# Kernel tuning notes

Measured on AMD Instinct MI355X. Metric: run time of the kernel, lower is better.

Reference implementation:

```python
import jax, jax.numpy as jnp
from jax import lax
import numpy as np

B, L, C = 16, 4096, 512
G = 8            # n_groups
CG = C // G      # group_dim = 64
WD = 4           # weather_dim
ORF = 10.0       # offset_range_factor


def conv1d(x, w, b=None):
    # x: [N, Cin, L], w: [Cout, Cin, 3], stride 1, padding 1
    y = lax.conv_general_dilated(x, w, window_strides=(1,), padding=[(1, 1)],
                                 dimension_numbers=('NCH', 'OIH', 'NCH'))
    if b is not None:
        y = y + b[None, :, None]
    return y


def group_norm(x, gamma, beta, groups=4, eps=1e-5):
    N, Cc, Ln = x.shape
    xr = x.reshape(N, groups, Cc // groups, Ln)
    mu = xr.mean(axis=(2, 3), keepdims=True)
    var = ((xr - mu) ** 2).mean(axis=(2, 3), keepdims=True)
    xn = ((xr - mu) / jnp.sqrt(var + eps)).reshape(N, Cc, Ln)
    return xn * gamma[None, :, None] + beta[None, :, None]


def grid_sample_bilinear_border(inp, grid):
    # Faithful torch F.grid_sample(mode='bilinear', padding_mode='border', align_corners=True)
    # inp: [N, C, H, W]; grid: [N, Ho, Wo, 2], grid[...,0]=x (width coord), grid[...,1]=y (height coord)
    N, Cc, H, W = inp.shape
    _, Ho, Wo, _ = grid.shape
    gx, gy = grid[..., 0], grid[..., 1]
    ix = jnp.clip((gx + 1.0) * 0.5 * (W - 1), 0.0, W - 1)  # border padding clamps coords
    iy = jnp.clip((gy + 1.0) * 0.5 * (H - 1), 0.0, H - 1)
    ix0f = jnp.floor(ix); iy0f = jnp.floor(iy)
    wx = ix - ix0f; wy = iy - iy0f
    ix0 = jnp.clip(ix0f.astype(jnp.int32), 0, W - 1)
    iy0 = jnp.clip(iy0f.astype(jnp.int32), 0, H - 1)
    ix1 = jnp.clip(ix0 + 1, 0, W - 1)
    iy1 = jnp.clip(iy0 + 1, 0, H - 1)
    flat = inp.reshape(N, Cc, H * W)
    def gather(iyk, ixk):
        idx = (iyk * W + ixk).reshape(N, 1, Ho * Wo)
        return jnp.take_along_axis(flat, idx, axis=2).reshape(N, Cc, Ho, Wo)
    v00 = gather(iy0, ix0); v01 = gather(iy0, ix1)
    v10 = gather(iy1, ix0); v11 = gather(iy1, ix1)
    wx = wx[:, None, :, :]; wy = wy[:, None, :, :]
    return (v00 * (1 - wy) * (1 - wx) + v01 * (1 - wy) * wx
            + v10 * wy * (1 - wx) + v11 * wy * wx)


def _forward(x, x_ext, w1, b1, gn_g, gn_b, w2, b2, w3, gate):
    xt = jnp.transpose(x, (0, 2, 1))              # [B, C, L]
    xg = xt.reshape(B * G, CG, L)                 # [B*G, CG, L]
    xe = jnp.transpose(x_ext, (0, 2, 1))          # [B, WD, L]
    xe = jnp.tile(xe, (G, 1, 1))                  # torch .repeat(n_groups,1,1)
    pin = jnp.concatenate([xg, xe], axis=1)       # [B*G, CG+WD, L]
    h = jax.nn.gelu(group_norm(conv1d(pin, w1, b1), gn_g, gn_b), approximate=False)
    h = jax.nn.gelu(conv1d(h, w2, b2), approximate=False)
    offset = jnp.tanh(conv1d(h, w3)) * ORF        # [B*G, 1, L]
    off_n = offset * (2.0 / (L - 1.0))
    ref = (jnp.linspace(0.5, L - 0.5, L, dtype=x.dtype) / (L - 1.0)) * 2.0 - 1.0
    grid_x = jnp.clip(ref[None, None, :, None] + off_n[..., None], -1.0, 1.0)  # [B*G,1,L,1]
    grid = jnp.concatenate([grid_x, jnp.zeros_like(grid_x)], axis=-1)
    grid = jnp.transpose(grid, (0, 2, 1, 3))      # [B*G, L, 1, 2]
    xs = grid_sample_bilinear_border(xg[..., None], grid)[..., 0]  # [B*G, CG, L]
    x_out = xg + jnp.tanh(gate) * xs
    x_out = x_out.reshape(B, C, L)
    return jnp.transpose(x_out, (0, 2, 1)), offset


def setup_inputs() -> dict:
    key = jax.random.key(0)
    ks = jax.random.split(key, 8)
    s = 0.05
    return {
        'x': jax.random.normal(ks[0], (B, L, C), jnp.float32),
        'x_ext': jax.random.normal(ks[1], (B, L, WD), jnp.float32),
        'w1': jax.random.normal(ks[2], (64, CG + WD, 3), jnp.float32) * s,
        'b1': jax.random.normal(ks[3], (64,), jnp.float32) * s,
        'gn_g': jnp.ones((64,), jnp.float32),
        'gn_b': jnp.zeros((64,), jnp.float32),
        'w2': jax.random.normal(ks[4], (32, 64, 3), jnp.float32) * s,
        'b2': jax.random.normal(ks[5], (32,), jnp.float32) * s,
        'w3': jax.random.normal(ks[6], (1, 32, 3), jnp.float32) * s,
        'gate': jnp.array([0.5], jnp.float32),
    }


def reference(x, x_ext, w1, b1, gn_g, gn_b, w2, b2, w3, gate):
    return _forward(x, x_ext, w1, b1, gn_g, gn_b, w2, b2, w3, gate)
```

## Files before the change

### kernel.cpp

```cpp
#include <hip/hip_runtime.h>
#include <hip/hip_bf16.h>

#define BB 16
#define LL 4096
#define CC 512
#define NG 128
#define IC1 68
#define OC1 64
#define OC2 32

typedef short short8 __attribute__((ext_vector_type(8)));
typedef float f32x4 __attribute__((ext_vector_type(4)));

__device__ inline ushort f2b(float f) {
    __hip_bfloat16 h = __float2bfloat16(f);
    return *reinterpret_cast<ushort*>(&h);
}
__device__ inline float b2f(ushort u) {
    __hip_bfloat16 h;
    *reinterpret_cast<ushort*>(&h) = u;
    return __bfloat162float(h);
}
__device__ inline float fast_tanh(float y) {
    float e = __expf(2.0f * y);
    return 1.0f - 2.0f / (e + 1.0f);
}
__device__ inline float fast_gelu(float x) {
    float y = x * (0.7978845608f + 0.0356774081f * x * x);
    return 0.5f * x * (1.0f + fast_tanh(y));
}

__global__ __launch_bounds__(256) void k_prep(const float* __restrict__ x,
    const float* __restrict__ w1, const float* __restrict__ w2,
    const float* __restrict__ gate,
    ushort* __restrict__ w1b, ushort* __restrict__ w2b, float* __restrict__ corr)
{
    int idx = blockIdx.x * 256 + threadIdx.x;
    if (idx < 18432) {
        int k = idx / 6144; int r = idx - k * 6144;
        int oc = r / 96;    int icp = r - oc * 96;
        float v = (icp < IC1) ? w1[(oc * IC1 + icp) * 3 + k] : 0.0f;
        w1b[idx] = f2b(v);
    } else if (idx < 24576) {
        int j = idx - 18432;
        int k = j / 2048; int r = j - k * 2048;
        int oc = r / 64;  int ic = r - oc * 64;
        w2b[j] = f2b(w2[(oc * OC1 + ic) * 3 + k]);
    } else if (idx < 32768) {
        int i3 = idx - 24576;
        int b = i3 >> 9; int ch = i3 & 511;
        float tg = tanhf(gate[0]);
        corr[i3] = tg * 0.5f *
            (x[((size_t)(b * LL + 2047)) * CC + ch] +
             x[((size_t)(b * LL + 2048)) * CC + ch]);
    }
}

#define KA_ROWS 66
#define KA_STR  104
template<bool FULL>
__device__ __forceinline__ void ka_body(ushort* pin,
    const float* __restrict__ x, const float* __restrict__ xe,
    const float* __restrict__ b1, const ushort* __restrict__ w1b,
    float* __restrict__ part, int n, int lt)
{
    const int b = n >> 3, g = n & 7, be = n & 15;
    const int l0 = lt * 64;
    const int t = threadIdx.x;
    const int q = t & 15;

    {
        const float* xb = &x[((size_t)b * LL + (l0 - 1)) * CC + g * 64 + q * 4];
#pragma unroll
        for (int i = 0; i < 9; ++i) {
            int pos = t + i * 128;
            if (pos < KA_ROWS * 16) {
                int li = pos >> 4;
                float4 v;
                if (FULL) {
                    v = *(const float4*)(xb + (size_t)li * CC);
                } else {
                    int l = l0 - 1 + li;
                    v = make_float4(0.f, 0.f, 0.f, 0.f);
                    if (l >= 0 && l < LL) v = *(const float4*)(xb + (size_t)li * CC);
                }
                uint lo = (uint)f2b(v.x) | ((uint)f2b(v.y) << 16);
                uint hi = (uint)f2b(v.z) | ((uint)f2b(v.w) << 16);
                *(uint2*)&pin[li * KA_STR + q * 4] = make_uint2(lo, hi);
            }
        }
    }
    if (t < KA_ROWS) {
        int l = l0 - 1 + t;
        float4 v = make_float4(0.f, 0.f, 0.f, 0.f);
        if (FULL || (l >= 0 && l < LL))
            v = *(const float4*)&xe[(size_t)(be * LL + l) * 4];
        uint lo = (uint)f2b(v.x) | ((uint)f2b(v.y) << 16);
        uint hi = (uint)f2b(v.z) | ((uint)f2b(v.w) << 16);
        *(uint2*)&pin[t * KA_STR + 64] = make_uint2(lo, hi);
    }
#pragma unroll
    for (int i = 0; i < 4; ++i) {
        int pos = t + i * 128;
        if (pos < KA_ROWS * 7) {
            int li = pos / 7, j = pos - li * 7;
            *(uint2*)&pin[li * KA_STR + 68 + j * 4] = make_uint2(0u, 0u);
        }
    }
    __syncthreads();

    const int lane = t & 63;
    const int w = t >> 6;
    const int m = lane & 15, h = lane >> 4;

    short8 fa[2][9];
#pragma unroll
    for (int mi = 0; mi < 2; ++mi)
#pragma unroll
        for (int k = 0; k < 3; ++k)
#pragma unroll
            for (int c = 0; c < 3; ++c)
                fa[mi][k * 3 + c] = *(const short8*)&w1b[
                    (size_t)(k * 64 + w * 32 + mi * 16 + m) * 96 + c * 32 + h * 8];

    f32x4 acc[2][4] = {};
#pragma unroll
    for (int tt = 0; tt < 4; ++tt) {
        const int rowbase = tt * 16 + m;
#pragma unroll
        for (int k = 0; k < 3; ++k) {
#pragma unroll
            for (int c = 0; c < 3; ++c) {
                short8 fb = *(const short8*)&pin[(rowbase + k) * KA_STR + c * 32 + h * 8];
                acc[0][tt] = __builtin_amdgcn_mfma_f32_16x16x32_bf16(fa[0][k * 3 + c], fb, acc[0][tt], 0, 0, 0);
                acc[1][tt] = __builtin_amdgcn_mfma_f32_16x16x32_bf16(fa[1][k * 3 + c], fb, acc[1][tt], 0, 0, 0);
            }
        }
    }

#pragma unroll
    for (int mi = 0; mi < 2; ++mi) {
        float bias[4];
#pragma unroll
        for (int r = 0; r < 4; ++r)
            bias[r] = b1[w * 32 + mi * 16 + h * 4 + r];
        float s1 = 0.f, s2 = 0.f;
#pragma unroll
        for (int tt = 0; tt < 4; ++tt) {
            float v0 = acc[mi][tt][0] + bias[0];
            float v1 = acc[mi][tt][1] + bias[1];
            float v2 = acc[mi][tt][2] + bias[2];
            float v3 = acc[mi][tt][3] + bias[3];
            s1 += v0 + v1 + v2 + v3;
            s2 += v0 * v0 + v1 * v1 + v2 * v2 + v3 * v3;
        }
#pragma unroll
        for (int off = 32; off > 0; off >>= 1) {
            s1 += __shfl_down(s1, off, 64);
            s2 += __shfl_down(s2, off, 64);
        }
        if (lane == 0) {
            int gidx = w * 2 + mi;
            part[(((size_t)n * 4 + gidx) * 64 + lt) * 2 + 0] = s1;
            part[(((size_t)n * 4 + gidx) * 64 + lt) * 2 + 1] = s2;
        }
    }
}

__global__ __launch_bounds__(128, 6) void ka_stats(const float* __restrict__ x,
    const float* __restrict__ xe, const float* __restrict__ b1,
    const ushort* __restrict__ w1b, float* __restrict__ part)
{
    __shared__ ushort pin[KA_ROWS * KA_STR];
    const int n = blockIdx.y, lt = blockIdx.x;
    if (lt >= 1 && lt <= 62)
        ka_body<true>(pin, x, xe, b1, w1b, part, n, lt);
    else
        ka_body<false>(pin, x, xe, b1, w1b, part, n, lt);
}

#define BT 60
#define XR 66
#define PINS 104
#define P2S  72
#define H2S  66
template<bool FULL>
__device__ __forceinline__ void kb_body(ushort* smem, float* sstats,
    const float* __restrict__ x, const float* __restrict__ xe,
    const float* __restrict__ b1, const ushort* __restrict__ w1b,
    const float* __restrict__ part, const float* __restrict__ gn_g,
    const float* __restrict__ gn_b, const float* __restrict__ b2,
    const ushort* __restrict__ w2b, const float* __restrict__ w3,
    const float* __restrict__ corr, float* __restrict__ out,
    float* __restrict__ offs, int n, int lt)
{
    ushort* pin = smem;
    ushort* p2  = smem;
    ushort* h2b = smem + 4752;
    const int b = n >> 3, g = n & 7, be = n & 15;
    const int l0 = lt * BT;
    const int t = threadIdx.x;
    const int lane = t & 63;
    const int w = t >> 6;

#pragma unroll
    for (int gg = 0; gg < 2; ++gg) {
        int gidx = w * 2 + gg;
        float2 p = *(const float2*)&part[(((size_t)n * 4 + gidx) * 64 + lane) * 2];
        float s1 = p.x, s2 = p.y;
#pragma unroll
        for (int off = 32; off > 0; off >>= 1) {
            s1 += __shfl_down(s1, off, 64);
            s2 += __shfl_down(s2, off, 64);
        }
        if (lane == 0) {
            float mean = s1 * (1.0f / 65536.0f);
            float var  = s2 * (1.0f / 65536.0f) - mean * mean;
            sstats[gidx * 2 + 0] = mean;
            sstats[gidx * 2 + 1] = 1.0f / sqrtf(var + 1e-5f);
        }
    }

    const int q = t & 15;
    {
        const float4 corrv = *(const float4*)&corr[(b << 9) + g * 64 + q * 4];
        const float* xb = &x[((size_t)b * LL + (l0 - 3)) * CC + g * 64 + q * 4];
        float* ob = &out[((size_t)b * LL + (l0 - 3)) * CC + g * 64 + q * 4];
#pragma unroll
        for (int i = 0; i < 9; ++i) {
            int pos = t + i * 128;
            if (pos < XR * 16) {
                int li = pos >> 4;
                float4 v;
                bool inr = true;
                if (FULL) {
                    v = *(const float4*)(xb + (size_t)li * CC);
                } else {
                    int l = l0 - 3 + li;
                    inr = (l >= 0 && l < LL);
                    v = make_float4(0.f, 0.f, 0.f, 0.f);
                    if (inr) v = *(const float4*)(xb + (size_t)li * CC);
                }
                if (li >= 3 && li < 3 + BT && inr) {
                    float4 o;
                    o.x = v.x + corrv.x; o.y = v.y + corrv.y;
                    o.z = v.z + corrv.z; o.w = v.w + corrv.w;
                    *(float4*)(ob + (size_t)li * CC) = o;
                }
                uint lo = (uint)f2b(v.x) | ((uint)f2b(v.y) << 16);
                uint hi = (uint)f2b(v.z) | ((uint)f2b(v.w) << 16);
                *(uint2*)&pin[li * PINS + q * 4] = make_uint2(lo, hi);
            }
        }
        if (t < XR) {
            int l = l0 - 3 + t;
            float4 v = make_float4(0.f, 0.f, 0.f, 0.f);
            if (FULL || (l >= 0 && l < LL))
                v = *(const float4*)&xe[(size_t)(be * LL + l) * 4];
            uint lo = (uint)f2b(v.x) | ((uint)f2b(v.y) << 16);
            uint hi = (uint)f2b(v.z) | ((uint)f2b(v.w) << 16);
            *(uint2*)&pin[t * PINS + 64] = make_uint2(lo, hi);
        }
#pragma unroll
        for (int i = 0; i < 4; ++i) {
            int pos = t + i * 128;
            if (pos < XR * 7) {
                int li = pos / 7, j = pos - li * 7;
                *(uint2*)&pin[li * PINS + 68 + j * 4] = make_uint2(0u, 0u);
            }
        }
    }
    __syncthreads();

    const int m = lane & 15, h = lane >> 4;

    short8 fa[2][9];
#pragma unroll
    for (int mi = 0; mi < 2; ++mi)
#pragma unroll
        for (int k = 0; k < 3; ++k)
#pragma unroll
            for (int c = 0; c < 3; ++c)
                fa[mi][k * 3 + c] = *(const short8*)&w1b[
                    (size_t)(k * 64 + w * 32 + mi * 16 + m) * 96 + c * 32 + h * 8];

    f32x4 acc[2][4] = {};
#pragma unroll
    for (int tt = 0; tt < 4; ++tt) {
        const int rowbase = tt * 16 + m;
#pragma unroll
        for (int k = 0; k < 3; ++k) {
#pragma unroll
            for (int c = 0; c < 3; ++c) {
                short8 fb = *(const short8*)&pin[(rowbase + k) * PINS + c * 32 + h * 8];
                acc[0][tt] = __builtin_amdgcn_mfma_f32_16x16x32_bf16(fa[0][k * 3 + c], fb, acc[0][tt], 0, 0, 0);
                acc[1][tt] = __builtin_amdgcn_mfma_f32_16x16x32_bf16(fa[1][k * 3 + c], fb, acc[1][tt], 0, 0, 0);
            }
        }
    }
    __syncthreads();

#pragma unroll
    for (int mi = 0; mi < 2; ++mi) {
        int gi = w * 2 + mi;
        float mean = sstats[gi * 2], istd = sstats[gi * 2 + 1];
        float A_[4], B_[4];
#pragma unroll
        for (int r = 0; r < 4; ++r) {
            int oc = w * 32 + mi * 16 + h * 4 + r;
            float ga = gn_g[oc];
            A_[r] = istd * ga;
            B_[r] = gn_b[oc] + (b1[oc] - mean) * A_[r];
        }
#pragma unroll
        for (int tt = 0; tt < 4; ++tt) {
            int p = tt * 16 + m;
            uint2 pk = make_uint2(0u, 0u);
            int l = l0 - 2 + p;
            if (FULL || (l >= 0 && l < LL)) {
                float v0 = fast_gelu(fmaf(acc[mi][tt][0], A_[0], B_[0]));
                float v1 = fast_gelu(fmaf(acc[mi][tt][1], A_[1], B_[1]));
                float v2 = fast_gelu(fmaf(acc[mi][tt][2], A_[2], B_[2]));
                float v3 = fast_gelu(fmaf(acc[mi][tt][3], A_[3], B_[3]));
                pk.x = (uint)f2b(v0) | ((uint)f2b(v1) << 16);
                pk.y = (uint)f2b(v2) | ((uint)f2b(v3) << 16);
            }
            *(uint2*)&p2[p * P2S + w * 32 + mi * 16 + h * 4] = pk;
        }
    }
    __syncthreads();

    short8 fa2[6];
#pragma unroll
    for (int k = 0; k < 3; ++k)
#pragma unroll
        for (int c = 0; c < 2; ++c)
            fa2[k * 2 + c] = *(const short8*)&w2b[
                (size_t)(k * 32 + w * 16 + m) * 64 + c * 32 + h * 8];

    float bias2[4];
#pragma unroll
    for (int r = 0; r < 4; ++r)
        bias2[r] = b2[w * 16 + h * 4 + r];

    f32x4 acc2[4] = {};
#pragma unroll
    for (int u = 0; u < 4; ++u) {
        const int jb = u * 16 + m;
#pragma unroll
        for (int k = 0; k < 3; ++k) {
#pragma unroll
            for (int c = 0; c < 2; ++c) {
                short8 fb = *(const short8*)&p2[(jb + k) * P2S + c * 32 + h * 8];
                acc2[u] = __builtin_amdgcn_mfma_f32_16x16x32_bf16(fa2[k * 2 + c], fb, acc2[u], 0, 0, 0);
            }
        }
    }
#pragma unroll
    for (int u = 0; u < 4; ++u) {
        int j = u * 16 + m;
        int lj = l0 - 1 + j;
#pragma unroll
        for (int r = 0; r < 4; ++r) {
            int oc = w * 16 + h * 4 + r;
            float v = 0.f;
            if (FULL || (lj >= 0 && lj < LL))
                v = fast_gelu(acc2[u][r] + bias2[r]);
            h2b[oc * H2S + j] = f2b(v);
        }
    }
    __syncthreads();

    if (t < 2 * BT) {
        int qq = t >> 1, half = t & 1;
        int ic0 = half * 16;
        float a = 0.f;
#pragma unroll
        for (int ic = 0; ic < 16; ++ic) {
            int icc = ic0 + ic;
            float v0 = b2f(h2b[icc * H2S + qq]);
            float v1 = b2f(h2b[icc * H2S + qq + 1]);
            float v2 = b2f(h2b[icc * H2S + qq + 2]);
            a = fmaf(w3[icc * 3 + 0], v0, a);
            a = fmaf(w3[icc * 3 + 1], v1, a);
            a = fmaf(w3[icc * 3 + 2], v2, a);
        }
        a += __shfl_xor(a, 1, 64);
        if (half == 0) {
            int l = l0 + qq;
            if (FULL || l < LL)
                offs[(size_t)n * LL + l] = fast_tanh(a) * 10.0f;
        }
    }
}

__global__ __launch_bounds__(128, 6) void kb_fused(const float* __restrict__ x,
    const float* __restrict__ xe, const float* __restrict__ b1,
    const ushort* __restrict__ w1b, const float* __restrict__ part,
    const float* __restrict__ gn_g, const float* __restrict__ gn_b,
    const float* __restrict__ b2, const ushort* __restrict__ w2b,
    const float* __restrict__ w3, const float* __restrict__ corr,
    float* __restrict__ out, float* __restrict__ offs)
{
    __shared__ ushort smem[6864];
    __shared__ float sstats[8];
    const int n = blockIdx.y, lt = blockIdx.x;
    if (lt >= 1 && lt <= 67)
        kb_body<true >(smem, sstats, x, xe, b1, w1b, part, gn_g, gn_b, b2, w2b, w3, corr, out, offs, n, lt);
    else
        kb_body<false>(smem, sstats, x, xe, b1, w1b, part, gn_g, gn_b, b2, w2b, w3, corr, out, offs, n, lt);
}

extern "C" void kernel_launch(void* const* d_in, const int* in_sizes, int n_in,
                              void* d_out, int out_size, void* d_ws, size_t ws_size,
                              hipStream_t stream)
{
    const float* x    = (const float*)d_in[0];
    const float* xext = (const float*)d_in[1];
    const float* w1   = (const float*)d_in[2];
    const float* b1   = (const float*)d_in[3];
    const float* gng  = (const float*)d_in[4];
    const float* gnb  = (const float*)d_in[5];
    const float* w2   = (const float*)d_in[6];
    const float* b2   = (const float*)d_in[7];
    const float* w3   = (const float*)d_in[8];
    const float* gate = (const float*)d_in[9];

    float* out  = (float*)d_out;
    float* offs = out + (size_t)BB * LL * CC;

    char* ws = (char*)d_ws;
    float* part = (float*)(ws);
    ushort* w1b = (ushort*)(ws + 262144);
    ushort* w2b = (ushort*)(ws + 299008);
    float* corr = (float*)(ws + 311296);

    k_prep<<<128, 256, 0, stream>>>(x, w1, w2, gate, w1b, w2b, corr);
    dim3 g1(64, NG);
    ka_stats<<<g1, 128, 0, stream>>>(x, xext, b1, w1b, part);
    dim3 g3(69, NG);
    kb_fused<<<g3, 128, 0, stream>>>(x, xext, b1, w1b, part, gng, gnb, b2, w2b,
                                     w3, corr, out, offs);
}
```

Measured before the change: 186.1 us.

## Write output and bf16 x copy in stats pass; read compact bf16 in fused pass

The stats kernel now covers 128 positions with 256 threads and, while loading x, also writes the residual output (x + corr) and a compact per-group bf16 copy of x to workspace. The fused kernel then reads that bf16 copy instead of re-reading fp32 x, and uses an XOR-swizzled LDS layout with separate storage for the weather channels. Moving the output write into the first pass and halving the second pass's x read volume is meant to cut global traffic. In exchange it adds an extra bf16 write and read through workspace, and relaxes the fused kernel's launch bounds.

Result: faster. 166.8 us (-10.4%).

```diff
diff --git a/kernel.cpp b/kernel.cpp
--- a/kernel.cpp
+++ b/kernel.cpp
@@ -56,24 +56,28 @@
     }
 }
 
-#define KA_ROWS 66
+#define KA_ROWS 130
 #define KA_STR  104
 template<bool FULL>
 __device__ __forceinline__ void ka_body(ushort* pin,
     const float* __restrict__ x, const float* __restrict__ xe,
     const float* __restrict__ b1, const ushort* __restrict__ w1b,
-    float* __restrict__ part, int n, int lt)
+    const float* __restrict__ corr, float* __restrict__ part,
+    float* __restrict__ out, ushort* __restrict__ xbf, int n, int lt)
 {
     const int b = n >> 3, g = n & 7, be = n & 15;
-    const int l0 = lt * 64;
+    const int l0 = lt * 128;
     const int t = threadIdx.x;
     const int q = t & 15;
 
     {
+        const float4 corrv = *(const float4*)&corr[(b << 9) + g * 64 + q * 4];
         const float* xb = &x[((size_t)b * LL + (l0 - 1)) * CC + g * 64 + q * 4];
+        float* ob = &out[((size_t)b * LL + (l0 - 1)) * CC + g * 64 + q * 4];
+        ushort* xbb = &xbf[((size_t)n * LL + (l0 - 1)) * 64 + q * 4];
 #pragma unroll
         for (int i = 0; i < 9; ++i) {
-            int pos = t + i * 128;
+            int pos = t + i * 256;
             if (pos < KA_ROWS * 16) {
                 int li = pos >> 4;
                 float4 v;
@@ -86,7 +90,15 @@
                 }
                 uint lo = (uint)f2b(v.x) | ((uint)f2b(v.y) << 16);
                 uint hi = (uint)f2b(v.z) | ((uint)f2b(v.w) << 16);
-                *(uint2*)&pin[li * KA_STR + q * 4] = make_uint2(lo, hi);
+                uint2 pk = make_uint2(lo, hi);
+                if (li >= 1 && li <= 128) {
+                    float4 o;
+                    o.x = v.x + corrv.x; o.y = v.y + corrv.y;
+                    o.z = v.z + corrv.z; o.w = v.w + corrv.w;
+                    *(float4*)(ob + (size_t)li * CC) = o;
+                    *(uint2*)(xbb + (size_t)li * 64) = pk;
+                }
+                *(uint2*)&pin[li * KA_STR + q * 4] = pk;
             }
         }
     }
@@ -101,7 +113,7 @@
     }
 #pragma unroll
     for (int i = 0; i < 4; ++i) {
-        int pos = t + i * 128;
+        int pos = t + i * 256;
         if (pos < KA_ROWS * 7) {
             int li = pos / 7, j = pos - li * 7;
             *(uint2*)&pin[li * KA_STR + 68 + j * 4] = make_uint2(0u, 0u);
@@ -111,6 +123,7 @@
 
     const int lane = t & 63;
     const int w = t >> 6;
+    const int och = w & 1, lh = w >> 1;
     const int m = lane & 15, h = lane >> 4;
 
     short8 fa[2][9];
@@ -121,12 +134,12 @@
 #pragma unroll
             for (int c = 0; c < 3; ++c)
                 fa[mi][k * 3 + c] = *(const short8*)&w1b[
-                    (size_t)(k * 64 + w * 32 + mi * 16 + m) * 96 + c * 32 + h * 8];
+                    (size_t)(k * 64 + och * 32 + mi * 16 + m) * 96 + c * 32 + h * 8];
 
     f32x4 acc[2][4] = {};
 #pragma unroll
     for (int tt = 0; tt < 4; ++tt) {
-        const int rowbase = tt * 16 + m;
+        const int rowbase = lh * 64 + tt * 16 + m;
 #pragma unroll
         for (int k = 0; k < 3; ++k) {
 #pragma unroll
@@ -143,7 +156,7 @@
         float bias[4];
 #pragma unroll
         for (int r = 0; r < 4; ++r)
-            bias[r] = b1[w * 32 + mi * 16 + h * 4 + r];
+            bias[r] = b1[och * 32 + mi * 16 + h * 4 + r];
         float s1 = 0.f, s2 = 0.f;
 #pragma unroll
         for (int tt = 0; tt < 4; ++tt) {
@@ -160,44 +173,44 @@
             s2 += __shfl_down(s2, off, 64);
         }
         if (lane == 0) {
-            int gidx = w * 2 + mi;
-            part[(((size_t)n * 4 + gidx) * 64 + lt) * 2 + 0] = s1;
-            part[(((size_t)n * 4 + gidx) * 64 + lt) * 2 + 1] = s2;
-        }
-    }
-}
-
-__global__ __launch_bounds__(128, 6) void ka_stats(const float* __restrict__ x,
+            int gidx = och * 2 + mi;
+            part[(((size_t)n * 4 + gidx) * 64 + lt * 2 + lh) * 2 + 0] = s1;
+            part[(((size_t)n * 4 + gidx) * 64 + lt * 2 + lh) * 2 + 1] = s2;
+        }
+    }
+}
+
+__global__ __launch_bounds__(256) void ka_stats(const float* __restrict__ x,
     const float* __restrict__ xe, const float* __restrict__ b1,
-    const ushort* __restrict__ w1b, float* __restrict__ part)
+    const ushort* __restrict__ w1b, const float* __restrict__ corr,
+    float* __restrict__ part, float* __restrict__ out, ushort* __restrict__ xbf)
 {
     __shared__ ushort pin[KA_ROWS * KA_STR];
     const int n = blockIdx.y, lt = blockIdx.x;
-    if (lt >= 1 && lt <= 62)
-        ka_body<true>(pin, x, xe, b1, w1b, part, n, lt);
+    if (lt >= 1 && lt <= 30)
+        ka_body<true>(pin, x, xe, b1, w1b, corr, part, out, xbf, n, lt);
     else
-        ka_body<false>(pin, x, xe, b1, w1b, part, n, lt);
+        ka_body<false>(pin, x, xe, b1, w1b, corr, part, out, xbf, n, lt);
 }
 
 #define BT 60
 #define XR 66
-#define PINS 104
 #define P2S  72
 #define H2S  66
 template<bool FULL>
 __device__ __forceinline__ void kb_body(ushort* smem, float* sstats,
-    const float* __restrict__ x, const float* __restrict__ xe,
-    const float* __restrict__ b1, const ushort* __restrict__ w1b,
-    const float* __restrict__ part, const float* __restrict__ gn_g,
+    const float* __restrict__ xe, const ushort* __restrict__ xbf,
+    const float* __restrict__ part, const float* __restrict__ b1,
+    const ushort* __restrict__ w1b, const float* __restrict__ gn_g,
     const float* __restrict__ gn_b, const float* __restrict__ b2,
     const ushort* __restrict__ w2b, const float* __restrict__ w3,
-    const float* __restrict__ corr, float* __restrict__ out,
     float* __restrict__ offs, int n, int lt)
 {
     ushort* pin = smem;
+    ushort* xeb = smem + 4224;
     ushort* p2  = smem;
     ushort* h2b = smem + 4752;
-    const int b = n >> 3, g = n & 7, be = n & 15;
+    const int be = n & 15;
     const int l0 = lt * BT;
     const int t = threadIdx.x;
     const int lane = t & 63;
@@ -221,54 +234,38 @@
         }
     }
 
-    const int q = t & 15;
     {
-        const float4 corrv = *(const float4*)&corr[(b << 9) + g * 64 + q * 4];
-        const float* xb = &x[((size_t)b * LL + (l0 - 3)) * CC + g * 64 + q * 4];
-        float* ob = &out[((size_t)b * LL + (l0 - 3)) * CC + g * 64 + q * 4];
-#pragma unroll
-        for (int i = 0; i < 9; ++i) {
-            int pos = t + i * 128;
-            if (pos < XR * 16) {
-                int li = pos >> 4;
-                float4 v;
-                bool inr = true;
+        const uint4* xs = (const uint4*)(xbf + ((size_t)n * LL + (l0 - 3)) * 64);
+#pragma unroll
+        for (int i = 0; i < 5; ++i) {
+            int s = t + i * 128;
+            if (s < XR * 8) {
+                int row = s >> 3, ch = s & 7;
+                uint4 v;
                 if (FULL) {
-                    v = *(const float4*)(xb + (size_t)li * CC);
+                    v = xs[s];
                 } else {
-                    int l = l0 - 3 + li;
-                    inr = (l >= 0 && l < LL);
-                    v = make_float4(0.f, 0.f, 0.f, 0.f);
-                    if (inr) v = *(const float4*)(xb + (size_t)li * CC);
+                    int l = l0 - 3 + row;
+                    v = make_uint4(0u, 0u, 0u, 0u);
+                    if (l >= 0 && l < LL) v = xs[s];
                 }
-                if (li >= 3 && li < 3 + BT && inr) {
-                    float4 o;
-                    o.x = v.x + corrv.x; o.y = v.y + corrv.y;
-                    o.z = v.z + corrv.z; o.w = v.w + corrv.w;
-                    *(float4*)(ob + (size_t)li * CC) = o;
-                }
-                uint lo = (uint)f2b(v.x) | ((uint)f2b(v.y) << 16);
-                uint hi = (uint)f2b(v.z) | ((uint)f2b(v.w) << 16);
-                *(uint2*)&pin[li * PINS + q * 4] = make_uint2(lo, hi);
-            }
-        }
-        if (t < XR) {
-            int l = l0 - 3 + t;
-            float4 v = make_float4(0.f, 0.f, 0.f, 0.f);
-            if (FULL || (l >= 0 && l < LL))
-                v = *(const float4*)&xe[(size_t)(be * LL + l) * 4];
-            uint lo = (uint)f2b(v.x) | ((uint)f2b(v.y) << 16);
-            uint hi = (uint)f2b(v.z) | ((uint)f2b(v.w) << 16);
-            *(uint2*)&pin[t * PINS + 64] = make_uint2(lo, hi);
-        }
-#pragma unroll
-        for (int i = 0; i < 4; ++i) {
-            int pos = t + i * 128;
-            if (pos < XR * 7) {
-                int li = pos / 7, j = pos - li * 7;
-                *(uint2*)&pin[li * PINS + 68 + j * 4] = make_uint2(0u, 0u);
-            }
-        }
+                ((uint4*)pin)[(row << 3) | (ch ^ (row & 7))] = v;
+            }
+        }
+    }
+    if (t < XR) {
+        int l = l0 - 3 + t;
+        float4 v = make_float4(0.f, 0.f, 0.f, 0.f);
+        if (FULL || (l >= 0 && l < LL))
+            v = *(const float4*)&xe[(size_t)(be * LL + l) * 4];
+        uint lo = (uint)f2b(v.x) | ((uint)f2b(v.y) << 16);
+        uint hi = (uint)f2b(v.z) | ((uint)f2b(v.w) << 16);
+        int sw = t & 3;
+        uint4 z = make_uint4(0u, 0u, 0u, 0u);
+        ((uint4*)xeb)[(t << 2) | (0 ^ sw)] = make_uint4(lo, hi, 0u, 0u);
+        ((uint4*)xeb)[(t << 2) | (1 ^ sw)] = z;
+        ((uint4*)xeb)[(t << 2) | (2 ^ sw)] = z;
+        ((uint4*)xeb)[(t << 2) | (3 ^ sw)] = z;
     }
     __syncthreads();
 
@@ -287,12 +284,17 @@
     f32x4 acc[2][4] = {};
 #pragma unroll
     for (int tt = 0; tt < 4; ++tt) {
-        const int rowbase = tt * 16 + m;
+        const int p = tt * 16 + m;
 #pragma unroll
         for (int k = 0; k < 3; ++k) {
+            const int row = p + k;
 #pragma unroll
             for (int c = 0; c < 3; ++c) {
-                short8 fb = *(const short8*)&pin[(rowbase + k) * PINS + c * 32 + h * 8];
+                short8 fb;
+                if (c < 2)
+                    fb = *(const short8*)&pin[(size_t)(((row << 3) | ((c * 4 + h) ^ (row & 7))) << 3)];
+                else
+                    fb = *(const short8*)&xeb[(size_t)(((row << 2) | (h ^ (row & 3))) << 3)];
                 acc[0][tt] = __builtin_amdgcn_mfma_f32_16x16x32_bf16(fa[0][k * 3 + c], fb, acc[0][tt], 0, 0, 0);
                 acc[1][tt] = __builtin_amdgcn_mfma_f32_16x16x32_bf16(fa[1][k * 3 + c], fb, acc[1][tt], 0, 0, 0);
             }
@@ -394,21 +396,20 @@
     }
 }
 
-__global__ __launch_bounds__(128, 6) void kb_fused(const float* __restrict__ x,
-    const float* __restrict__ xe, const float* __restrict__ b1,
-    const ushort* __restrict__ w1b, const float* __restrict__ part,
+__global__ __launch_bounds__(128, 4) void kb_fused(const float* __restrict__ xe,
+    const ushort* __restrict__ xbf, const float* __restrict__ part,
+    const float* __restrict__ b1, const ushort* __restrict__ w1b,
     const float* __restrict__ gn_g, const float* __restrict__ gn_b,
     const float* __restrict__ b2, const ushort* __restrict__ w2b,
-    const float* __restrict__ w3, const float* __restrict__ corr,
-    float* __restrict__ out, float* __restrict__ offs)
+    const float* __restrict__ w3, float* __restrict__ offs)
 {
     __shared__ ushort smem[6864];
     __shared__ float sstats[8];
     const int n = blockIdx.y, lt = blockIdx.x;
     if (lt >= 1 && lt <= 67)
-        kb_body<true >(smem, sstats, x, xe, b1, w1b, part, gn_g, gn_b, b2, w2b, w3, corr, out, offs, n, lt);
+        kb_body<true >(smem, sstats, xe, xbf, part, b1, w1b, gn_g, gn_b, b2, w2b, w3, offs, n, lt);
     else
-        kb_body<false>(smem, sstats, x, xe, b1, w1b, part, gn_g, gn_b, b2, w2b, w3, corr, out, offs, n, lt);
+        kb_body<false>(smem, sstats, xe, xbf, part, b1, w1b, gn_g, gn_b, b2, w2b, w3, offs, n, lt);
 }
 
 extern "C" void kernel_launch(void* const* d_in, const int* in_sizes, int n_in,
@@ -434,11 +435,12 @@
     ushort* w1b = (ushort*)(ws + 262144);
     ushort* w2b = (ushort*)(ws + 299008);
     float* corr = (float*)(ws + 311296);
+    ushort* xbf = (ushort*)(ws + 344064);
 
     k_prep<<<128, 256, 0, stream>>>(x, w1, w2, gate, w1b, w2b, corr);
-    dim3 g1(64, NG);
-    ka_stats<<<g1, 128, 0, stream>>>(x, xext, b1, w1b, part);
+    dim3 g1(32, NG);
+    ka_stats<<<g1, 256, 0, stream>>>(x, xext, b1, w1b, corr, part, out, xbf);
     dim3 g3(69, NG);
-    kb_fused<<<g3, 128, 0, stream>>>(x, xext, b1, w1b, part, gng, gnb, b2, w2b,
-                                     w3, corr, out, offs);
-}
+    kb_fused<<<g3, 128, 0, stream>>>(xext, xbf, part, b1, w1b, gng, gnb, b2, w2b,
+                                     w3, offs);
+}
```
